# Optimization experiments

Measured on AMD Instinct MI355X. Metric: run time of the kernel, lower is better.

The kernel has to match this reference:

```python
import jax, jax.numpy as jnp
import numpy as np

B, N, D, H = 8, 1025, 768, 12
PRE = 1            # prefix (CLS) tokens
P = N - PRE        # patch tokens
HD = D // H
EPS = 1e-6


def setup_inputs() -> dict:
    key = jax.random.key(0)
    ks = jax.random.split(key, 8)
    x = jax.random.normal(ks[0], (B, N, D), dtype=jnp.float32)
    graph = jax.random.uniform(ks[1], (B, P, P), dtype=jnp.float32)
    transferability = jax.random.uniform(ks[2], (B, P), dtype=jnp.float32)
    Wqkv = jax.random.normal(ks[3], (3 * D, D), dtype=jnp.float32) * 0.02
    bqkv = jnp.zeros((3 * D,), dtype=jnp.float32)
    Wproj = jax.random.normal(ks[4], (D, D), dtype=jnp.float32) * 0.02
    bproj = jnp.zeros((D,), dtype=jnp.float32)
    return {"x": x, "graph": graph, "transferability": transferability,
            "Wqkv": Wqkv, "bqkv": bqkv, "Wproj": Wproj, "bproj": bproj,
            "prefix_tokens": PRE}


def _build_mask(graph, transferability, prefix_tokens, n_tokens):
    # patch_weights: [B, P]
    pw = transferability / (jnp.sum(transferability, axis=1, keepdims=True) + EPS)
    b, p = pw.shape
    pre = prefix_tokens
    # Block layout: [[1s (pre,pre), pw broadcast (pre,P)], [pw[:,None] (P,pre), graph]]
    top_left = jnp.ones((b, pre, pre), dtype=graph.dtype)
    top_right = jnp.broadcast_to(pw[:, None, :], (b, pre, p))
    bot_left = jnp.broadcast_to(pw[:, :, None], (b, p, pre))
    top = jnp.concatenate([top_left, top_right], axis=2)
    bot = jnp.concatenate([bot_left, graph], axis=2)
    return jnp.concatenate([top, bot], axis=1)  # [B, N, N]


def reference(x, graph, transferability, Wqkv, bqkv, Wproj, bproj, prefix_tokens):
    bsz, n, d = x.shape
    scale = HD ** -0.5
    qkv = x @ Wqkv.T + bqkv                          # [B, N, 3D]
    qkv = qkv.reshape(bsz, n, 3, H, HD).transpose(2, 0, 3, 1, 4)  # [3, B, H, N, hd]
    q, k, v = qkv[0], qkv[1], qkv[2]
    attn = jax.nn.softmax(jnp.einsum('bhid,bhjd->bhij', q, k) * scale, axis=-1)
    mask = _build_mask(graph, transferability, prefix_tokens, n)  # [B, N, N]
    attn = attn * mask[:, None, :, :]
    attn = attn / (jnp.sum(attn, axis=-1, keepdims=True) + EPS)
    out = jnp.einsum('bhij,bhjd->bhid', attn, v)     # [B, H, N, hd]
    out = out.transpose(0, 2, 1, 3).reshape(bsz, n, d)
    return out @ Wproj.T + bproj
```

## Files before the change

### kernel.cpp

```cpp
#include <hip/hip_runtime.h>
#include <stdint.h>

constexpr int Bq = 8, Nn = 1025, Dd = 768, Hh = 12, HDd = 64, Pp = 1024;
constexpr int NP = 1088;
constexpr int MROWS = Bq * Nn;
constexpr float EPSI = 1e-6f;

typedef __attribute__((ext_vector_type(8))) short bfrag;
typedef __attribute__((ext_vector_type(4))) short bfrag4;
typedef __attribute__((ext_vector_type(4))) float ffrag;
typedef __attribute__((ext_vector_type(4))) float f4;
typedef __attribute__((ext_vector_type(4))) unsigned short us4;

#define MFMA16(a, b, c) __builtin_amdgcn_mfma_f32_16x16x32_bf16((a), (b), (c), 0, 0, 0)

__device__ __forceinline__ ffrag MFMA16K16(bfrag4 a, bfrag4 b, ffrag c) {
#if __has_builtin(__builtin_amdgcn_mfma_f32_16x16x16bf16_1k)
  return __builtin_amdgcn_mfma_f32_16x16x16bf16_1k(a, b, c, 0, 0, 0);
#else
  asm volatile("v_mfma_f32_16x16x16_bf16 %0, %1, %2, %0" : "+v"(c) : "v"(a), "v"(b));
  return c;
#endif
}

#if __has_builtin(__builtin_amdgcn_exp2f)
#define EXP2(x) __builtin_amdgcn_exp2f(x)
#else
#define EXP2(x) exp2f(x)
#endif

__device__ __forceinline__ unsigned short f2bf(float f) {
  union { float f; uint32_t u; } v{f};
  uint32_t u = v.u;
  return (unsigned short)((u + 0x7fffu + ((u >> 16) & 1u)) >> 16);
}
__device__ __forceinline__ float bf2f(unsigned short s) {
  union { uint32_t u; float f; } v; v.u = ((uint32_t)s) << 16; return v.f;
}
__device__ __forceinline__ uint32_t pkbf(float a, float b) {
  uint32_t r;
  asm("v_cvt_pk_bf16_f32 %0, %1, %2" : "=v"(r) : "v"(a), "v"(b));
  return r;
}

__device__ __forceinline__ void gload16(const void* g, void* l) {
  __builtin_amdgcn_global_load_lds((const __attribute__((address_space(1))) unsigned int*)g,
                                   (__attribute__((address_space(3))) unsigned int*)l, 16, 0, 0);
}

__global__ __launch_bounds__(256) void conv3_kernel(const float* __restrict__ s0, unsigned short* __restrict__ d0, int n0,
                                                    const float* __restrict__ s1, unsigned short* __restrict__ d1, int n1,
                                                    const float* __restrict__ s2, unsigned short* __restrict__ d2, int n2) {
  int idx = blockIdx.x * blockDim.x + threadIdx.x;
  int stride = gridDim.x * blockDim.x;
  int ntot = n0 + n1 + n2;
  for (int i = idx; i < ntot; i += stride) {
    const float* src; unsigned short* dst; int k;
    if (i < n0) { src = s0; dst = d0; k = i; }
    else if (i < n0 + n1) { src = s1; dst = d1; k = i - n0; }
    else { src = s2; dst = d2; k = i - n0 - n1; }
    f4 v = ((const f4*)src)[k];
    us4 o; o[0] = f2bf(v[0]); o[1] = f2bf(v[1]); o[2] = f2bf(v[2]); o[3] = f2bf(v[3]);
    ((us4*)dst)[k] = o;
  }
}

__global__ __launch_bounds__(256) void pw_kernel(const float* __restrict__ tr, float* __restrict__ pw) {
  int b = blockIdx.x;
  __shared__ float red[256];
  float s = 0.f;
  for (int j = threadIdx.x; j < Pp; j += 256) s += tr[b * Pp + j];
  red[threadIdx.x] = s; __syncthreads();
  for (int o = 128; o > 0; o >>= 1) { if (threadIdx.x < o) red[threadIdx.x] += red[threadIdx.x + o]; __syncthreads(); }
  float inv = 1.f / (red[0] + EPSI);
  for (int j = threadIdx.x; j < Pp; j += 256) pw[b * Pp + j] = tr[b * Pp + j] * inv;
}

__global__ __launch_bounds__(256) void mask_kernel(const float* __restrict__ graph,
                                                   const float* __restrict__ pw,
                                                   unsigned short* __restrict__ mask) {
  int i = blockIdx.x, b = blockIdx.y;
  int t = threadIdx.x;
  unsigned short* mrow = mask + ((size_t)b * NP + i) * NP;
  if (i >= Nn) {
    for (int j = t; j < NP; j += 256) mrow[j] = 0;
    return;
  }
  const float* src = (i == 0) ? (pw + b * Pp) : (graph + ((size_t)b * Pp + (i - 1)) * Pp);
  f4 v = ((const f4*)src)[t];
  int j = 1 + 4 * t;
  mrow[j]     = f2bf(v[0]);
  mrow[j + 1] = f2bf(v[1]);
  mrow[j + 2] = f2bf(v[2]);
  mrow[j + 3] = f2bf(v[3]);
  if (t == 0) mrow[0] = (i == 0) ? f2bf(1.f) : f2bf(pw[b * Pp + i - 1]);
  for (int jj = Nn + t; jj < NP; jj += 256) mrow[jj] = 0;
}

__global__ __launch_bounds__(256) void padzero_kernel(unsigned short* __restrict__ Qo,
                                                      unsigned short* __restrict__ Ko,
                                                      unsigned short* __restrict__ Vo) {
  int bh = blockIdx.x;
  unsigned short* qp = Qo + ((size_t)bh * NP + Nn) * 64;
  unsigned short* kp = Ko + ((size_t)bh * NP + Nn) * 64;
  for (int idx = threadIdx.x; idx < (NP - Nn) * 64; idx += 256) { qp[idx] = 0; kp[idx] = 0; }
  unsigned short* vp = Vo + (size_t)bh * 64 * NP;
  for (int idx = threadIdx.x; idx < 64 * (NP - Nn); idx += 256) {
    int d = idx / (NP - Nn), j = Nn + (idx - d * (NP - Nn));
    vp[(size_t)d * NP + j] = 0;
  }
}

__device__ __forceinline__ void gemm_main(const unsigned short* __restrict__ A, int rowA0, int rowAmax,
                                          const unsigned short* __restrict__ Bw, int rowB0,
                                          uint4* lds, ffrag acc[4][4], int tid) {
  const int l = tid & 63, lm = l & 15, lg = l >> 4, w = tid >> 6, wr = w >> 1, wc = w & 1;
  const unsigned short* aS[4]; const unsigned short* bS[4];
#pragma unroll
  for (int q = 0; q < 4; q++) {
    int c = tid + 256 * q, r = c >> 3, p = c & 7, g = p ^ (r & 7);
    int ra = rowA0 + r; if (ra > rowAmax) ra = rowAmax;
    aS[q] = A + (size_t)ra * 768 + 8 * g;
    bS[q] = Bw + (size_t)(rowB0 + r) * 768 + 8 * g;
  }
  uint4* buf0 = lds;
  uint4* buf1 = lds + 2048;
#pragma unroll
  for (int q = 0; q < 4; q++) {
    gload16(aS[q], buf0 + tid + 256 * q);
    gload16(bS[q], buf0 + 1024 + tid + 256 * q);
    aS[q] += 64; bS[q] += 64;
  }
  asm volatile("s_waitcnt vmcnt(0)" ::: "memory");
  __builtin_amdgcn_sched_barrier(0);
  __builtin_amdgcn_s_barrier();
#pragma unroll 1
  for (int kt = 0; kt < 12; kt++) {
    uint4* cur = (kt & 1) ? buf1 : buf0;
    uint4* nxt = (kt & 1) ? buf0 : buf1;
    if (kt < 11) {
#pragma unroll
      for (int q = 0; q < 4; q++) {
        gload16(aS[q], nxt + tid + 256 * q);
        gload16(bS[q], nxt + 1024 + tid + 256 * q);
        aS[q] += 64; bS[q] += 64;
      }
    }
    const bfrag* LA = (const bfrag*)cur;
    const bfrag* LB = (const bfrag*)(cur + 1024);
    bfrag af[4][2], bf_[4][2];
#pragma unroll
    for (int am = 0; am < 4; am++) {
      int row = wr * 64 + am * 16 + lm;
      af[am][0] = LA[row * 8 + ((0 + lg) ^ (row & 7))];
      af[am][1] = LA[row * 8 + ((4 + lg) ^ (row & 7))];
    }
#pragma unroll
    for (int an = 0; an < 4; an++) {
      int row = wc * 64 + an * 16 + lm;
      bf_[an][0] = LB[row * 8 + ((0 + lg) ^ (row & 7))];
      bf_[an][1] = LB[row * 8 + ((4 + lg) ^ (row & 7))];
    }
#pragma unroll
    for (int am = 0; am < 4; am++)
#pragma unroll
      for (int an = 0; an < 4; an++) {
        acc[am][an] = MFMA16(af[am][0], bf_[an][0], acc[am][an]);
        acc[am][an] = MFMA16(af[am][1], bf_[an][1], acc[am][an]);
      }
    asm volatile("s_waitcnt vmcnt(0)" ::: "memory");
    __builtin_amdgcn_sched_barrier(0);
    __builtin_amdgcn_s_barrier();
  }
}

__device__ __forceinline__ int xcd_chunk_map(int orig, int nwg) {
  int qq = nwg >> 3, rr = nwg & 7;
  int xcd = orig & 7, idx = orig >> 3;
  int base = (xcd < rr) ? xcd * (qq + 1) : rr * (qq + 1) + (xcd - rr) * qq;
  return base + idx;
}

__global__ __launch_bounds__(256) void qkv_gemm_kernel(const unsigned short* __restrict__ X,
                                                       const unsigned short* __restrict__ W,
                                                       const float* __restrict__ bias,
                                                       unsigned short* __restrict__ Qo,
                                                       unsigned short* __restrict__ Ko,
                                                       unsigned short* __restrict__ Vo) {
  __shared__ uint4 lds[4096];
  int tid = threadIdx.x;
  int wg = xcd_chunk_map(blockIdx.x, 65 * 18);
  int xt = wg / 18, yt = wg - 18 * xt;
  ffrag zero4 = {0.f, 0.f, 0.f, 0.f};
  ffrag acc[4][4];
#pragma unroll
  for (int i = 0; i < 4; i++)
#pragma unroll
    for (int j = 0; j < 4; j++) acc[i][j] = zero4;
  gemm_main(X, xt * 128, MROWS - 1, W, yt * 128, lds, acc, tid);
  const int l = tid & 63, lm = l & 15, lg = l >> 4, w = tid >> 6, wr = w >> 1, wc = w & 1;
#pragma unroll
  for (int an = 0; an < 4; an++) {
    int gc = yt * 128 + wc * 64 + an * 16 + lm;
    int which = gc / 768, rr = gc - which * 768, h = rr >> 6, hd = rr & 63;
    float bv = bias[gc];
#pragma unroll
    for (int am = 0; am < 4; am++) {
      int grb = xt * 128 + wr * 64 + am * 16 + 4 * lg;
#pragma unroll
      for (int r = 0; r < 4; r++) {
        int gr = grb + r;
        if (gr >= MROWS) continue;
        int b = gr / Nn, i = gr - b * Nn;
        size_t bh = (size_t)(b * Hh + h);
        float v = acc[am][an][r] + bv;
        if (which == 0)      Qo[(bh * NP + i) * 64 + hd] = f2bf(v * 0.18033688f);
        else if (which == 1) Ko[(bh * NP + i) * 64 + hd] = f2bf(v);
        else                 Vo[(bh * 64 + hd) * NP + i] = f2bf(v);
      }
    }
  }
}

__global__ __launch_bounds__(256) void proj_gemm_kernel(const unsigned short* __restrict__ A,
                                                        const unsigned short* __restrict__ W,
                                                        const float* __restrict__ bias,
                                                        float* __restrict__ out) {
  __shared__ uint4 lds[4096];
  int tid = threadIdx.x;
  int wg = xcd_chunk_map(blockIdx.x, 65 * 6);
  int xt = wg / 6, yt = wg - 6 * xt;
  ffrag zero4 = {0.f, 0.f, 0.f, 0.f};
  ffrag acc[4][4];
#pragma unroll
  for (int i = 0; i < 4; i++)
#pragma unroll
    for (int j = 0; j < 4; j++) acc[i][j] = zero4;
  gemm_main(A, xt * 128, MROWS - 1, W, yt * 128, lds, acc, tid);
  const int l = tid & 63, lm = l & 15, lg = l >> 4, w = tid >> 6, wr = w >> 1, wc = w & 1;
#pragma unroll
  for (int an = 0; an < 4; an++) {
    int gc = yt * 128 + wc * 64 + an * 16 + lm;
    float bv = bias[gc];
#pragma unroll
    for (int am = 0; am < 4; am++) {
      int grb = xt * 128 + wr * 64 + am * 16 + 4 * lg;
#pragma unroll
      for (int r = 0; r < 4; r++) {
        int gr = grb + r;
        if (gr >= MROWS) continue;
        out[(size_t)gr * 768 + gc] = acc[am][an][r] + bv;
      }
    }
  }
}

__global__ __launch_bounds__(256) void attn_kernel(const unsigned short* __restrict__ Qg,
                                                   const unsigned short* __restrict__ Kg,
                                                   const unsigned short* __restrict__ Vg,
                                                   const unsigned short* __restrict__ Mg,
                                                   unsigned short* __restrict__ Og) {
  __shared__ uint4 smem[2048];
  int tid = threadIdx.x, w = tid >> 6, l = tid & 63, lm = l & 15, lg = l >> 4;
  int bx = blockIdx.x;
  int b = bx & 7, t5 = bx >> 3;
  int h = t5 % 12, ib = t5 / 12;
  size_t bh = (size_t)(b * Hh + h);
  const unsigned short* Qb = Qg + bh * NP * 64;
  const unsigned short* Kb = Kg + bh * NP * 64;
  const unsigned short* Vb = Vg + bh * 64 * NP;
  int i0a = ib * 128 + w * 16;
  int i0b = i0a + 64;
  int irowa = i0a + lm; if (irowa > NP - 1) irowa = NP - 1;
  int irowb = i0b + lm; if (irowb > NP - 1) irowb = NP - 1;
  const unsigned short* Mrowa = Mg + (size_t)b * NP * NP + (size_t)irowa * NP;
  const unsigned short* Mrowb = Mg + (size_t)b * NP * NP + (size_t)irowb * NP;

  bfrag qa0 = *(const bfrag*)(Qb + (size_t)irowa * 64 + 8 * lg);
  bfrag qa1 = *(const bfrag*)(Qb + (size_t)irowa * 64 + 32 + 8 * lg);
  bfrag qb0 = *(const bfrag*)(Qb + (size_t)irowb * 64 + 8 * lg);
  bfrag qb1 = *(const bfrag*)(Qb + (size_t)irowb * 64 + 32 + 8 * lg);

  ffrag zero4 = {0.f, 0.f, 0.f, 0.f};
  ffrag oaccA[4] = {zero4, zero4, zero4, zero4};
  ffrag oaccB[4] = {zero4, zero4, zero4, zero4};
  float TpA = 0.f, TpB = 0.f;

  int rS = tid >> 3, pS = tid & 7;
  int rS2 = rS + 32;
  const unsigned short* kS0 = Kb + (size_t)rS * 64 + 8 * (pS ^ (rS & 7));
  const unsigned short* kS1 = Kb + (size_t)rS2 * 64 + 8 * (pS ^ (rS2 & 7));
  const unsigned short* vS0 = Vb + (size_t)rS * NP + 8 * (pS ^ (rS & 7));
  const unsigned short* vS1 = Vb + (size_t)rS2 * NP + 8 * (pS ^ (rS2 & 7));

  gload16(kS0, smem + tid);
  gload16(kS1, smem + tid + 256);
  gload16(vS0, smem + 512 + tid);
  gload16(vS1, smem + 512 + tid + 256);
  asm volatile("s_waitcnt vmcnt(0)" ::: "memory");
  __builtin_amdgcn_sched_barrier(0);
  __builtin_amdgcn_s_barrier();

#pragma unroll 1
  for (int t = 0; t < 17; t++) {
    int cb = (t & 1) << 10;
    int j0 = t * 64;
    us4 mvA[4], mvB[4];
#pragma unroll
    for (int jm = 0; jm < 4; jm++) {
      mvA[jm] = *(const us4*)(Mrowa + j0 + 16 * jm + 4 * lg);
      mvB[jm] = *(const us4*)(Mrowb + j0 + 16 * jm + 4 * lg);
    }
    __builtin_amdgcn_sched_barrier(0);
    if (t < 16) {
      int nb = ((t + 1) & 1) << 10;
      size_t ko = (size_t)(t + 1) * 4096;
      int vo = (t + 1) * 64;
      gload16(kS0 + ko, smem + nb + tid);
      gload16(kS1 + ko, smem + nb + tid + 256);
      gload16(vS0 + vo, smem + nb + 512 + tid);
      gload16(vS1 + vo, smem + nb + 512 + tid + 256);
    }
    __builtin_amdgcn_sched_barrier(0);
    const bfrag* LK = (const bfrag*)(smem + cb);
    const char*  LVc = (const char*)(smem + cb + 512);

    bfrag ka[4], kb2[4];
#pragma unroll
    for (int jm = 0; jm < 4; jm++) {
      int row = jm * 16 + lm;
      ka[jm]  = LK[row * 8 + ((0 + lg) ^ (row & 7))];
      kb2[jm] = LK[row * 8 + ((4 + lg) ^ (row & 7))];
    }
    ffrag sa[4], sb[4];
    __builtin_amdgcn_s_setprio(1);
#pragma unroll
    for (int jm = 0; jm < 4; jm++) {
      ffrag a = zero4;
      a = MFMA16(ka[jm], qa0, a);
      a = MFMA16(kb2[jm], qa1, a);
      sa[jm] = a;
      ffrag bb = zero4;
      bb = MFMA16(ka[jm], qb0, bb);
      bb = MFMA16(kb2[jm], qb1, bb);
      sb[jm] = bb;
    }
    __builtin_amdgcn_s_setprio(0);

    bfrag4 vf[4][4];
#pragma unroll
    for (int jm = 0; jm < 4; jm++)
#pragma unroll
      for (int dm = 0; dm < 4; dm++) {
        int vrow = dm * 16 + lm;
        union { uint2 u; bfrag4 b; } cu;
        cu.u = *(const uint2*)(LVc + vrow * 128 +
                               ((((jm << 1) | (lg >> 1)) ^ (vrow & 7)) << 4) + 8 * (lg & 1));
        vf[jm][dm] = cu.b;
      }

    bfrag4 paA[4], paB[4];
#pragma unroll
    for (int jm = 0; jm < 4; jm++) {
      float p0 = EXP2(sa[jm][0]), p1 = EXP2(sa[jm][1]), p2 = EXP2(sa[jm][2]), p3 = EXP2(sa[jm][3]);
      float q0 = p0 * bf2f(mvA[jm][0]), q1 = p1 * bf2f(mvA[jm][1]);
      float q2 = p2 * bf2f(mvA[jm][2]), q3 = p3 * bf2f(mvA[jm][3]);
      TpA += (q0 + q1) + (q2 + q3);
      union { uint2 u; bfrag4 b; } cv;
      cv.u.x = pkbf(q0, q1); cv.u.y = pkbf(q2, q3);
      paA[jm] = cv.b;
    }
#pragma unroll
    for (int jm = 0; jm < 4; jm++) {
      float p0 = EXP2(sb[jm][0]), p1 = EXP2(sb[jm][1]), p2 = EXP2(sb[jm][2]), p3 = EXP2(sb[jm][3]);
      float q0 = p0 * bf2f(mvB[jm][0]), q1 = p1 * bf2f(mvB[jm][1]);
      float q2 = p2 * bf2f(mvB[jm][2]), q3 = p3 * bf2f(mvB[jm][3]);
      TpB += (q0 + q1) + (q2 + q3);
      union { uint2 u; bfrag4 b; } cv;
      cv.u.x = pkbf(q0, q1); cv.u.y = pkbf(q2, q3);
      paB[jm] = cv.b;
    }

    __builtin_amdgcn_s_setprio(1);
#pragma unroll
    for (int jm = 0; jm < 4; jm++)
#pragma unroll
      for (int dm = 0; dm < 4; dm++) {
        oaccA[dm] = MFMA16K16(paA[jm], vf[jm][dm], oaccA[dm]);
        oaccB[dm] = MFMA16K16(paB[jm], vf[jm][dm], oaccB[dm]);
      }
    __builtin_amdgcn_s_setprio(0);

    asm volatile("s_waitcnt vmcnt(0)" ::: "memory");
    __builtin_amdgcn_sched_barrier(0);
    __builtin_amdgcn_s_barrier();
  }
  TpA += __shfl_xor(TpA, 16); TpA += __shfl_xor(TpA, 32);
  TpB += __shfl_xor(TpB, 16); TpB += __shfl_xor(TpB, 32);
  float dnA_row = 1.f / TpA;
  float dnB_row = 1.f / TpB;
  float dnA[4], dnB[4];
#pragma unroll
  for (int r = 0; r < 4; r++) { dnA[r] = __shfl(dnA_row, 4 * lg + r); dnB[r] = __shfl(dnB_row, 4 * lg + r); }
#pragma unroll
  for (int dm = 0; dm < 4; dm++)
#pragma unroll
    for (int r = 0; r < 4; r++) {
      int ia = i0a + 4 * lg + r;
      if (ia < Nn) Og[((size_t)(b * Nn + ia)) * Dd + h * 64 + dm * 16 + lm] = f2bf(oaccA[dm][r] * dnA[r]);
      int ibr = i0b + 4 * lg + r;
      if (ibr < Nn) Og[((size_t)(b * Nn + ibr)) * Dd + h * 64 + dm * 16 + lm] = f2bf(oaccB[dm][r] * dnB[r]);
    }
}

extern "C" void kernel_launch(void* const* d_in, const int* in_sizes, int n_in,
                              void* d_out, int out_size, void* d_ws, size_t ws_size,
                              hipStream_t stream) {
  const float* x      = (const float*)d_in[0];
  const float* graph  = (const float*)d_in[1];
  const float* transf = (const float*)d_in[2];
  const float* Wqkv   = (const float*)d_in[3];
  const float* bqkv   = (const float*)d_in[4];
  const float* Wproj  = (const float*)d_in[5];
  const float* bproj  = (const float*)d_in[6];
  float* out = (float*)d_out;
  char* ws = (char*)d_ws;

  unsigned short* xbf  = (unsigned short*)(ws + 0);
  unsigned short* wqb  = (unsigned short*)(ws + 12595200);
  unsigned short* wpb  = (unsigned short*)(ws + 16134144);
  unsigned short* Qb   = (unsigned short*)(ws + 17313792);
  unsigned short* Kb   = (unsigned short*)(ws + 30683136);
  unsigned short* Vb   = (unsigned short*)(ws + 44052480);
  float*          pw   = (float*)(ws + 57421824);
  unsigned short* mask = (unsigned short*)(ws + 57454592);
  unsigned short* aob  = xbf;

  conv3_kernel<<<2048, 256, 0, stream>>>(x, xbf, (MROWS * Dd) / 4,
                                         Wqkv, wqb, (3 * Dd * Dd) / 4,
                                         Wproj, wpb, (Dd * Dd) / 4);
  pw_kernel<<<Bq, 256, 0, stream>>>(transf, pw);
  mask_kernel<<<dim3(NP, Bq), 256, 0, stream>>>(graph, pw, mask);
  padzero_kernel<<<96, 256, 0, stream>>>(Qb, Kb, Vb);
  qkv_gemm_kernel<<<65 * 18, 256, 0, stream>>>(xbf, wqb, bqkv, Qb, Kb, Vb);
  attn_kernel<<<864, 256, 0, stream>>>(Qb, Kb, Vb, mask, aob);
  proj_gemm_kernel<<<65 * 6, 256, 0, stream>>>(aob, wpb, bproj, out);
}
```

Before: 199.3 us.

## Split attention KV range across waves with per-wave staging and cross-wave reduction

Restructures the attention kernel so each block handles 64 query rows, and each of its four waves processes a different 16-key slice of every 64-key tile. Each wave stages its own K/V slice into private LDS double buffers, so block-wide barriers inside the loop are no longer needed. Partial outputs and row sums are combined through shared memory at the end. The grid grows from 864 to 1632 blocks to raise parallelism, at the cost of a tree reduction epilogue, more syncthreads, and more redundant mask and Q loads.

```diff
diff --git a/kernel.cpp b/kernel.cpp
--- a/kernel.cpp
+++ b/kernel.cpp
@@ -260,7 +260,7 @@
                                                    const unsigned short* __restrict__ Vg,
                                                    const unsigned short* __restrict__ Mg,
                                                    unsigned short* __restrict__ Og) {
-  __shared__ uint4 smem[2048];
+  __shared__ uint4 smem[2112];
   int tid = threadIdx.x, w = tid >> 6, l = tid & 63, lm = l & 15, lg = l >> 4;
   int bx = blockIdx.x;
   int b = bx & 7, t5 = bx >> 3;
@@ -269,148 +269,179 @@
   const unsigned short* Qb = Qg + bh * NP * 64;
   const unsigned short* Kb = Kg + bh * NP * 64;
   const unsigned short* Vb = Vg + bh * 64 * NP;
-  int i0a = ib * 128 + w * 16;
-  int i0b = i0a + 64;
-  int irowa = i0a + lm; if (irowa > NP - 1) irowa = NP - 1;
-  int irowb = i0b + lm; if (irowb > NP - 1) irowb = NP - 1;
-  const unsigned short* Mrowa = Mg + (size_t)b * NP * NP + (size_t)irowa * NP;
-  const unsigned short* Mrowb = Mg + (size_t)b * NP * NP + (size_t)irowb * NP;
-
-  bfrag qa0 = *(const bfrag*)(Qb + (size_t)irowa * 64 + 8 * lg);
-  bfrag qa1 = *(const bfrag*)(Qb + (size_t)irowa * 64 + 32 + 8 * lg);
-  bfrag qb0 = *(const bfrag*)(Qb + (size_t)irowb * 64 + 8 * lg);
-  bfrag qb1 = *(const bfrag*)(Qb + (size_t)irowb * 64 + 32 + 8 * lg);
+  int q0 = ib * 64;
+
+  bfrag qf[4][2];
+  const unsigned short* Mrow[4];
+#pragma unroll
+  for (int qg = 0; qg < 4; qg++) {
+    int qr = q0 + qg * 16 + lm; if (qr > NP - 1) qr = NP - 1;
+    qf[qg][0] = *(const bfrag*)(Qb + (size_t)qr * 64 + 8 * lg);
+    qf[qg][1] = *(const bfrag*)(Qb + (size_t)qr * 64 + 32 + 8 * lg);
+    Mrow[qg] = Mg + (size_t)b * NP * NP + (size_t)qr * NP;
+  }
 
   ffrag zero4 = {0.f, 0.f, 0.f, 0.f};
-  ffrag oaccA[4] = {zero4, zero4, zero4, zero4};
-  ffrag oaccB[4] = {zero4, zero4, zero4, zero4};
-  float TpA = 0.f, TpB = 0.f;
-
-  int rS = tid >> 3, pS = tid & 7;
-  int rS2 = rS + 32;
-  const unsigned short* kS0 = Kb + (size_t)rS * 64 + 8 * (pS ^ (rS & 7));
-  const unsigned short* kS1 = Kb + (size_t)rS2 * 64 + 8 * (pS ^ (rS2 & 7));
-  const unsigned short* vS0 = Vb + (size_t)rS * NP + 8 * (pS ^ (rS & 7));
-  const unsigned short* vS1 = Vb + (size_t)rS2 * NP + 8 * (pS ^ (rS2 & 7));
-
-  gload16(kS0, smem + tid);
-  gload16(kS1, smem + tid + 256);
-  gload16(vS0, smem + 512 + tid);
-  gload16(vS1, smem + 512 + tid + 256);
+  ffrag oacc[4][4];
+#pragma unroll
+  for (int qg = 0; qg < 4; qg++)
+#pragma unroll
+    for (int dm = 0; dm < 4; dm++) oacc[qg][dm] = zero4;
+  float Tpart[4] = {0.f, 0.f, 0.f, 0.f};
+
+  uint4* mybuf = smem + w * 512;
+
+  auto STAGE = [&](int t, int bsel) {
+    int jb = t * 64 + w * 16;
+    uint4* dst = mybuf + bsel * 256;
+    {
+      int s = l, row = s >> 3, p = s & 7;
+      gload16(Kb + (size_t)(jb + row) * 64 + 8 * (p ^ (row & 7)), dst + s);
+    }
+    {
+      int s = l + 64, row = s >> 3, p = s & 7;
+      gload16(Kb + (size_t)(jb + row) * 64 + 8 * (p ^ (row & 7)), dst + s);
+    }
+    {
+      int s = l, d = s >> 1, hf = s & 1;
+      gload16(Vb + (size_t)d * NP + jb + 8 * hf, dst + 128 + s);
+    }
+    {
+      int s = l + 64, d = s >> 1, hf = s & 1;
+      gload16(Vb + (size_t)d * NP + jb + 8 * hf, dst + 128 + s);
+    }
+  };
+
+  STAGE(0, 0);
   asm volatile("s_waitcnt vmcnt(0)" ::: "memory");
   __builtin_amdgcn_sched_barrier(0);
-  __builtin_amdgcn_s_barrier();
 
 #pragma unroll 1
   for (int t = 0; t < 17; t++) {
-    int cb = (t & 1) << 10;
-    int j0 = t * 64;
-    us4 mvA[4], mvB[4];
-#pragma unroll
-    for (int jm = 0; jm < 4; jm++) {
-      mvA[jm] = *(const us4*)(Mrowa + j0 + 16 * jm + 4 * lg);
-      mvB[jm] = *(const us4*)(Mrowb + j0 + 16 * jm + 4 * lg);
-    }
+    int bsel = t & 1;
+    int jb = t * 64 + w * 16;
+    us4 mv[4];
+#pragma unroll
+    for (int qg = 0; qg < 4; qg++) mv[qg] = *(const us4*)(Mrow[qg] + jb + 4 * lg);
     __builtin_amdgcn_sched_barrier(0);
-    if (t < 16) {
-      int nb = ((t + 1) & 1) << 10;
-      size_t ko = (size_t)(t + 1) * 4096;
-      int vo = (t + 1) * 64;
-      gload16(kS0 + ko, smem + nb + tid);
-      gload16(kS1 + ko, smem + nb + tid + 256);
-      gload16(vS0 + vo, smem + nb + 512 + tid);
-      gload16(vS1 + vo, smem + nb + 512 + tid + 256);
-    }
+    if (t < 16) STAGE(t + 1, bsel ^ 1);
     __builtin_amdgcn_sched_barrier(0);
-    const bfrag* LK = (const bfrag*)(smem + cb);
-    const char*  LVc = (const char*)(smem + cb + 512);
-
-    bfrag ka[4], kb2[4];
-#pragma unroll
-    for (int jm = 0; jm < 4; jm++) {
-      int row = jm * 16 + lm;
-      ka[jm]  = LK[row * 8 + ((0 + lg) ^ (row & 7))];
-      kb2[jm] = LK[row * 8 + ((4 + lg) ^ (row & 7))];
-    }
-    ffrag sa[4], sb[4];
+    if (t < 16) { asm volatile("s_waitcnt vmcnt(4)" ::: "memory"); }
+    else        { asm volatile("s_waitcnt vmcnt(0)" ::: "memory"); }
+    __builtin_amdgcn_sched_barrier(0);
+
+    const bfrag* LK = (const bfrag*)(mybuf + bsel * 256);
+    const char*  LV = (const char*)(mybuf + bsel * 256 + 128);
+
+    bfrag ka0 = LK[lm * 8 + ((0 + lg) ^ (lm & 7))];
+    bfrag ka1 = LK[lm * 8 + ((4 + lg) ^ (lm & 7))];
+
+    ffrag s4[4];
     __builtin_amdgcn_s_setprio(1);
 #pragma unroll
-    for (int jm = 0; jm < 4; jm++) {
+    for (int qg = 0; qg < 4; qg++) {
       ffrag a = zero4;
-      a = MFMA16(ka[jm], qa0, a);
-      a = MFMA16(kb2[jm], qa1, a);
-      sa[jm] = a;
-      ffrag bb = zero4;
-      bb = MFMA16(ka[jm], qb0, bb);
-      bb = MFMA16(kb2[jm], qb1, bb);
-      sb[jm] = bb;
+      a = MFMA16(ka0, qf[qg][0], a);
+      a = MFMA16(ka1, qf[qg][1], a);
+      s4[qg] = a;
     }
     __builtin_amdgcn_s_setprio(0);
 
-    bfrag4 vf[4][4];
-#pragma unroll
-    for (int jm = 0; jm < 4; jm++)
+    bfrag4 pa[4];
+#pragma unroll
+    for (int qg = 0; qg < 4; qg++) {
+      float p0 = EXP2(s4[qg][0]), p1 = EXP2(s4[qg][1]), p2 = EXP2(s4[qg][2]), p3 = EXP2(s4[qg][3]);
+      float q0f = p0 * bf2f(mv[qg][0]), q1f = p1 * bf2f(mv[qg][1]);
+      float q2f = p2 * bf2f(mv[qg][2]), q3f = p3 * bf2f(mv[qg][3]);
+      Tpart[qg] += (q0f + q1f) + (q2f + q3f);
+      union { uint2 u; bfrag4 bb; } cv;
+      cv.u.x = pkbf(q0f, q1f); cv.u.y = pkbf(q2f, q3f);
+      pa[qg] = cv.bb;
+    }
+
+    __builtin_amdgcn_s_setprio(1);
+#pragma unroll
+    for (int dm = 0; dm < 4; dm++) {
+      union { uint2 u; bfrag4 bb; } cu;
+      cu.u = *(const uint2*)(LV + (dm * 16 + lm) * 32 + lg * 8);
+      bfrag4 vf = cu.bb;
+#pragma unroll
+      for (int qg = 0; qg < 4; qg++) oacc[qg][dm] = MFMA16K16(pa[qg], vf, oacc[qg][dm]);
+    }
+    __builtin_amdgcn_s_setprio(0);
+  }
+
+#pragma unroll
+  for (int qg = 0; qg < 4; qg++) {
+    Tpart[qg] += __shfl_xor(Tpart[qg], 16);
+    Tpart[qg] += __shfl_xor(Tpart[qg], 32);
+  }
+  float* Tred = (float*)(smem + 2048);
+  if (l < 16) {
+#pragma unroll
+    for (int qg = 0; qg < 4; qg++) Tred[w * 64 + qg * 16 + l] = Tpart[qg];
+  }
+  __syncthreads();
+  float dnr[4];
+#pragma unroll
+  for (int qg = 0; qg < 4; qg++) {
+    float s = (Tred[qg * 16 + lm] + Tred[64 + qg * 16 + lm]) +
+              (Tred[128 + qg * 16 + lm] + Tred[192 + qg * 16 + lm]);
+    dnr[qg] = 1.f / s;
+  }
+  float dn[4][4];
+#pragma unroll
+  for (int qg = 0; qg < 4; qg++)
+#pragma unroll
+    for (int r = 0; r < 4; r++) dn[qg][r] = __shfl(dnr[qg], 4 * lg + r);
+
+  uint4* A0 = smem;
+  uint4* A1 = smem + 1024;
+  if (w == 1) {
+#pragma unroll
+    for (int qg = 0; qg < 4; qg++)
+#pragma unroll
+      for (int dm = 0; dm < 4; dm++) *(ffrag*)(A0 + (qg * 4 + dm) * 64 + l) = oacc[qg][dm];
+  } else if (w == 3) {
+#pragma unroll
+    for (int qg = 0; qg < 4; qg++)
+#pragma unroll
+      for (int dm = 0; dm < 4; dm++) *(ffrag*)(A1 + (qg * 4 + dm) * 64 + l) = oacc[qg][dm];
+  }
+  __syncthreads();
+  if (w == 0) {
+#pragma unroll
+    for (int qg = 0; qg < 4; qg++)
+#pragma unroll
+      for (int dm = 0; dm < 4; dm++) oacc[qg][dm] += *(const ffrag*)(A0 + (qg * 4 + dm) * 64 + l);
+  } else if (w == 2) {
+#pragma unroll
+    for (int qg = 0; qg < 4; qg++)
+#pragma unroll
+      for (int dm = 0; dm < 4; dm++) oacc[qg][dm] += *(const ffrag*)(A1 + (qg * 4 + dm) * 64 + l);
+  }
+  __syncthreads();
+  if (w == 2) {
+#pragma unroll
+    for (int qg = 0; qg < 4; qg++)
+#pragma unroll
+      for (int dm = 0; dm < 4; dm++) *(ffrag*)(A0 + (qg * 4 + dm) * 64 + l) = oacc[qg][dm];
+  }
+  __syncthreads();
+  if (w == 0) {
+#pragma unroll
+    for (int qg = 0; qg < 4; qg++)
 #pragma unroll
       for (int dm = 0; dm < 4; dm++) {
-        int vrow = dm * 16 + lm;
-        union { uint2 u; bfrag4 b; } cu;
-        cu.u = *(const uint2*)(LVc + vrow * 128 +
-                               ((((jm << 1) | (lg >> 1)) ^ (vrow & 7)) << 4) + 8 * (lg & 1));
-        vf[jm][dm] = cu.b;
+        oacc[qg][dm] += *(const ffrag*)(A0 + (qg * 4 + dm) * 64 + l);
+#pragma unroll
+        for (int r = 0; r < 4; r++) {
+          int q = q0 + qg * 16 + 4 * lg + r;
+          if (q < Nn)
+            Og[((size_t)(b * Nn + q)) * Dd + h * 64 + dm * 16 + lm] = f2bf(oacc[qg][dm][r] * dn[qg][r]);
+        }
       }
-
-    bfrag4 paA[4], paB[4];
-#pragma unroll
-    for (int jm = 0; jm < 4; jm++) {
-      float p0 = EXP2(sa[jm][0]), p1 = EXP2(sa[jm][1]), p2 = EXP2(sa[jm][2]), p3 = EXP2(sa[jm][3]);
-      float q0 = p0 * bf2f(mvA[jm][0]), q1 = p1 * bf2f(mvA[jm][1]);
-      float q2 = p2 * bf2f(mvA[jm][2]), q3 = p3 * bf2f(mvA[jm][3]);
-      TpA += (q0 + q1) + (q2 + q3);
-      union { uint2 u; bfrag4 b; } cv;
-      cv.u.x = pkbf(q0, q1); cv.u.y = pkbf(q2, q3);
-      paA[jm] = cv.b;
-    }
-#pragma unroll
-    for (int jm = 0; jm < 4; jm++) {
-      float p0 = EXP2(sb[jm][0]), p1 = EXP2(sb[jm][1]), p2 = EXP2(sb[jm][2]), p3 = EXP2(sb[jm][3]);
-      float q0 = p0 * bf2f(mvB[jm][0]), q1 = p1 * bf2f(mvB[jm][1]);
-      float q2 = p2 * bf2f(mvB[jm][2]), q3 = p3 * bf2f(mvB[jm][3]);
-      TpB += (q0 + q1) + (q2 + q3);
-      union { uint2 u; bfrag4 b; } cv;
-      cv.u.x = pkbf(q0, q1); cv.u.y = pkbf(q2, q3);
-      paB[jm] = cv.b;
-    }
-
-    __builtin_amdgcn_s_setprio(1);
-#pragma unroll
-    for (int jm = 0; jm < 4; jm++)
-#pragma unroll
-      for (int dm = 0; dm < 4; dm++) {
-        oaccA[dm] = MFMA16K16(paA[jm], vf[jm][dm], oaccA[dm]);
-        oaccB[dm] = MFMA16K16(paB[jm], vf[jm][dm], oaccB[dm]);
-      }
-    __builtin_amdgcn_s_setprio(0);
-
-    asm volatile("s_waitcnt vmcnt(0)" ::: "memory");
-    __builtin_amdgcn_sched_barrier(0);
-    __builtin_amdgcn_s_barrier();
-  }
-  TpA += __shfl_xor(TpA, 16); TpA += __shfl_xor(TpA, 32);
-  TpB += __shfl_xor(TpB, 16); TpB += __shfl_xor(TpB, 32);
-  float dnA_row = 1.f / TpA;
-  float dnB_row = 1.f / TpB;
-  float dnA[4], dnB[4];
-#pragma unroll
-  for (int r = 0; r < 4; r++) { dnA[r] = __shfl(dnA_row, 4 * lg + r); dnB[r] = __shfl(dnB_row, 4 * lg + r); }
-#pragma unroll
-  for (int dm = 0; dm < 4; dm++)
-#pragma unroll
-    for (int r = 0; r < 4; r++) {
-      int ia = i0a + 4 * lg + r;
-      if (ia < Nn) Og[((size_t)(b * Nn + ia)) * Dd + h * 64 + dm * 16 + lm] = f2bf(oaccA[dm][r] * dnA[r]);
-      int ibr = i0b + 4 * lg + r;
-      if (ibr < Nn) Og[((size_t)(b * Nn + ibr)) * Dd + h * 64 + dm * 16 + lm] = f2bf(oaccB[dm][r] * dnB[r]);
-    }
+  }
 }
 
 extern "C" void kernel_launch(void* const* d_in, const int* in_sizes, int n_in,
@@ -443,6 +474,6 @@
   mask_kernel<<<dim3(NP, Bq), 256, 0, stream>>>(graph, pw, mask);
   padzero_kernel<<<96, 256, 0, stream>>>(Qb, Kb, Vb);
   qkv_gemm_kernel<<<65 * 18, 256, 0, stream>>>(xbf, wqb, bqkv, Qb, Kb, Vb);
-  attn_kernel<<<864, 256, 0, stream>>>(Qb, Kb, Vb, mask, aob);
+  attn_kernel<<<1632, 256, 0, stream>>>(Qb, Kb, Vb, mask, aob);
   proj_gemm_kernel<<<65 * 6, 256, 0, stream>>>(aob, wpb, bproj, out);
 }
```

New measurement: 224.3 us. 12.5% more time.
